# Kernel optimization log

Measured on AMD Instinct MI355X. Metric: run time of the kernel, lower is better.

Reference implementation:

```python
import jax, jax.numpy as jnp
import numpy as np

HEADS = 4
DIM_U = 1
DIM_K = 16
DIM_V = 32  # dim_out // heads = 128 // 4
EPS = 1e-5


def setup_inputs() -> dict:
    key = jax.random.key(0)
    ks = jax.random.split(key, 9)
    b, dim, hh, ww = 16, 256, 32, 32
    n = m = hh * ww
    x = jax.random.normal(ks[0], (b, dim, hh, ww), dtype=jnp.float32)
    # 1x1 conv weights (out_ch, in_ch), kaiming-ish scale
    s = 1.0 / np.sqrt(dim)
    w_q = jax.random.normal(ks[1], (DIM_K * HEADS, dim), dtype=jnp.float32) * s
    w_k = jax.random.normal(ks[2], (DIM_K * DIM_U, dim), dtype=jnp.float32) * s
    w_v = jax.random.normal(ks[3], (DIM_V * DIM_U, dim), dtype=jnp.float32) * s
    pos_emb = jax.random.normal(ks[4], (n, m, DIM_K, DIM_U), dtype=jnp.float32)
    gamma_q = jnp.ones((DIM_K * HEADS,), dtype=jnp.float32)
    beta_q = jnp.zeros((DIM_K * HEADS,), dtype=jnp.float32)
    gamma_v = jnp.ones((DIM_V * DIM_U,), dtype=jnp.float32)
    beta_v = jnp.zeros((DIM_V * DIM_U,), dtype=jnp.float32)
    return {"x": x, "w_q": w_q, "w_k": w_k, "w_v": w_v, "pos_emb": pos_emb,
            "gamma_q": gamma_q, "beta_q": beta_q, "gamma_v": gamma_v, "beta_v": beta_v}


def _bn(t, gamma, beta):
    # BatchNorm2d in training mode: batch statistics over (b, h, w), biased var
    mean = t.mean(axis=(0, 2, 3), keepdims=True)
    var = t.var(axis=(0, 2, 3), keepdims=True)
    t = (t - mean) * jax.lax.rsqrt(var + EPS)
    return t * gamma[None, :, None, None] + beta[None, :, None, None]


def reference(x, w_q, w_k, w_v, pos_emb, gamma_q, beta_q, gamma_v, beta_v):
    b, c, hh, ww = x.shape
    h, u, dk, dv = HEADS, DIM_U, DIM_K, DIM_V
    # 1x1 convs == channel contractions
    q = jnp.einsum('oc,bcxy->boxy', w_q, x)
    k = jnp.einsum('oc,bcxy->boxy', w_k, x)
    v = jnp.einsum('oc,bcxy->boxy', w_v, x)
    q = _bn(q, gamma_q, beta_q)
    v = _bn(v, gamma_v, beta_v)
    n = hh * ww
    q = q.reshape(b, h, dk, n)        # b h k n
    k = k.reshape(b, dk, u, n)        # b k u m
    v = v.reshape(b, dv, u, n)        # b v u m
    k = jax.nn.softmax(k, axis=-1)
    lam_c = jnp.einsum('bkum,bvum->bkv', k, v)            # content lambda
    lam_p = jnp.einsum('nmku,bvum->bnkv', pos_emb, v)     # position lambdas
    Yc = jnp.einsum('bhkn,bkv->bnhv', q, lam_c)
    Yp = jnp.einsum('bhkn,bnkv->bnhv', q, lam_p)
    Y = Yc + Yp                                           # b n h v
    out = Y.transpose(0, 2, 3, 1).reshape(b, h * dv, hh, ww)
    return out
```

## Files before the change

### kernel.cpp

```cpp
#include <hip/hip_runtime.h>
#include <hip/hip_bf16.h>
#include <cstdint>


typedef __attribute__((ext_vector_type(8))) __bf16 bf16x8;
typedef __attribute__((ext_vector_type(4))) float f32x4;

__device__ __forceinline__ unsigned short f2bf(float f) {
    unsigned u = __float_as_uint(f);
    u += 0x7fffu + ((u >> 16) & 1u);
    return (unsigned short)(u >> 16);
}
__device__ __forceinline__ unsigned pk2(float a, float b) {
    return (unsigned)f2bf(a) | ((unsigned)f2bf(b) << 16);
}
__device__ __forceinline__ float bf2f(unsigned short h) {
    return __uint_as_float(((unsigned)h) << 16);
}
__device__ __forceinline__ void async16(const void* g, void* l) {
    __builtin_amdgcn_global_load_lds(
        (const __attribute__((address_space(1))) void*)g,
        (__attribute__((address_space(3))) void*)l, 16, 0, 0);
}

__global__ __launch_bounds__(256) void k_proj(const float* __restrict__ x,
                                              const float* __restrict__ wq,
                                              const float* __restrict__ wk,
                                              const float* __restrict__ wv,
                                              float* __restrict__ qraw,
                                              float* __restrict__ kraw,
                                              float* __restrict__ vraw) {
    int b = blockIdx.y;
    int px0 = blockIdx.x * 32;
    int t = threadIdx.x;
    int w = t >> 6, lane = t & 63;

    __shared__ __align__(16) unsigned short Al[128 * 32];
    __shared__ __align__(16) unsigned short Bl[32 * 34];

    int ch = t >> 1, half = t & 1;
    const float* wsrc = nullptr;
    if (ch < 64)       wsrc = wq + ch * 256;
    else if (ch < 80)  wsrc = wk + (ch - 64) * 256;
    else if (ch < 112) wsrc = wv + (ch - 80) * 256;
    if (wsrc) wsrc += half * 16;
    int s2 = (ch >> 1) & 3;
    unsigned short* wdst0 = &Al[ch * 32 + (((half * 2) ^ s2) << 3)];
    unsigned short* wdst1 = &Al[ch * 32 + (((half * 2 + 1) ^ s2) << 3)];

    int wm = w >> 1, wn = w & 1;
    int rl = lane & 15, qq = lane >> 4;
    int sw = qq ^ ((rl >> 1) & 3);

    f32x4 acc[4];
#pragma unroll
    for (int i = 0; i < 4; ++i)
#pragma unroll
        for (int r = 0; r < 4; ++r) acc[i][r] = 0.f;

    const float* xb = x + (size_t)b * 262144 + px0;

    for (int kt = 0; kt < 8; ++kt) {
        int c0 = kt * 32;
        {
            uint4 d0, d1;
            if (wsrc) {
                float4 f0 = *(const float4*)(wsrc + c0);
                float4 f1 = *(const float4*)(wsrc + c0 + 4);
                float4 f2 = *(const float4*)(wsrc + c0 + 8);
                float4 f3 = *(const float4*)(wsrc + c0 + 12);
                d0.x = pk2(f0.x, f0.y); d0.y = pk2(f0.z, f0.w);
                d0.z = pk2(f1.x, f1.y); d0.w = pk2(f1.z, f1.w);
                d1.x = pk2(f2.x, f2.y); d1.y = pk2(f2.z, f2.w);
                d1.z = pk2(f3.x, f3.y); d1.w = pk2(f3.z, f3.w);
            } else {
                d0 = make_uint4(0, 0, 0, 0); d1 = d0;
            }
            *(uint4*)wdst0 = d0;
            *(uint4*)wdst1 = d1;
        }
#pragma unroll
        for (int rep = 0; rep < 2; ++rep) {
            int idx = rep * 256 + t;
            int px = idx & 31;
            int cp = idx >> 5;
            int c = c0 + cp * 2;
            float f0 = xb[(size_t)c * 1024 + px];
            float f1 = xb[(size_t)(c + 1) * 1024 + px];
            *(unsigned*)&Bl[px * 34 + cp * 2] = pk2(f0, f1);
        }
        __syncthreads();
        bf16x8 a[4], bb;
#pragma unroll
        for (int i = 0; i < 4; ++i) a[i] = *(const bf16x8*)&Al[((wm << 6) + (i << 4) + rl) * 32 + sw * 8];
        bb = *(const bf16x8*)&Bl[((wn << 4) + rl) * 34 + qq * 8];
#pragma unroll
        for (int i = 0; i < 4; ++i)
            acc[i] = __builtin_amdgcn_mfma_f32_16x16x32_bf16(a[i], bb, acc[i], 0, 0, 0);
        __syncthreads();
    }

#pragma unroll
    for (int i = 0; i < 4; ++i) {
        int px = px0 + (wn << 4) + rl;
#pragma unroll
        for (int r = 0; r < 4; ++r) {
            int c = (wm << 6) + (i << 4) + (qq << 2) + r;
            float val = acc[i][r];
            if (c < 64)       qraw[((size_t)b * 64 + c) * 1024 + px] = val;
            else if (c < 80)  kraw[((size_t)b * 16 + (c - 64)) * 1024 + px] = val;
            else if (c < 112) vraw[((size_t)b * 32 + (c - 80)) * 1024 + px] = val;
        }
    }
}

__global__ __launch_bounds__(1024) void k_mid(const float* __restrict__ qraw,
                                              const float* __restrict__ kraw,
                                              const float* __restrict__ vraw,
                                              const float* __restrict__ gq, const float* __restrict__ bq,
                                              const float* __restrict__ gv, const float* __restrict__ bv,
                                              unsigned short* __restrict__ vbn,
                                              float* __restrict__ scaleArr, float* __restrict__ shiftArr,
                                              float* __restrict__ lamcraw) {
    int bx = blockIdx.x;
    int t = threadIdx.x;
    int w = t >> 6, lane = t & 63;
    __shared__ float redA[16], redB[16];
    __shared__ float bc[2];
    __shared__ float pr[16][32];

    if (bx < 96) {
        int ch = bx;
        const float* base;
        size_t bstride;
        if (ch < 64) { base = qraw + (size_t)ch * 1024; bstride = 65536; }
        else         { base = vraw + (size_t)(ch - 64) * 1024; bstride = 32768; }
        float s = 0.f, ss = 0.f;
#pragma unroll
        for (int b = 0; b < 16; ++b) { float v = base[b * bstride + t]; s += v; ss += v * v; }
#pragma unroll
        for (int off = 32; off; off >>= 1) { s += __shfl_down(s, off); ss += __shfl_down(ss, off); }
        if (lane == 0) { redA[w] = s; redB[w] = ss; }
        __syncthreads();
        if (t == 0) {
            s = 0.f; ss = 0.f;
#pragma unroll
            for (int i = 0; i < 16; ++i) { s += redA[i]; ss += redB[i]; }
            float mean = s * (1.f / 16384.f);
            float var = ss * (1.f / 16384.f) - mean * mean;
            float g, be;
            if (ch < 64) { g = gq[ch]; be = bq[ch]; } else { g = gv[ch - 64]; be = bv[ch - 64]; }
            float sc = g * rsqrtf(var + 1e-5f);
            float sh = be - mean * sc;
            scaleArr[ch] = sc; shiftArr[ch] = sh;
            bc[0] = sc; bc[1] = sh;
        }
        __syncthreads();
        if (ch >= 64) {
            float sc = bc[0], sh = bc[1];
            int vch = ch - 64;
#pragma unroll
            for (int b = 0; b < 16; ++b) {
                size_t idx = ((size_t)b * 32 + vch) * 1024 + t;
                vbn[idx] = f2bf(vraw[idx] * sc + sh);
            }
        }
    } else {
        int idx = bx - 96;
        int b = idx >> 4, kch = idx & 15;
        float xv = kraw[((size_t)b * 16 + kch) * 1024 + t];
        float mx = xv;
#pragma unroll
        for (int off = 32; off; off >>= 1) mx = fmaxf(mx, __shfl_down(mx, off));
        if (lane == 0) redA[w] = mx;
        __syncthreads();
        mx = redA[0];
#pragma unroll
        for (int i = 1; i < 16; ++i) mx = fmaxf(mx, redA[i]);
        float e = __expf(xv - mx);
        float s = e;
#pragma unroll
        for (int off = 32; off; off >>= 1) s += __shfl_down(s, off);
        __syncthreads();
        if (lane == 0) redB[w] = s;
        __syncthreads();
        s = 0.f;
#pragma unroll
        for (int i = 0; i < 16; ++i) s += redB[i];
        float inv = 1.f / s;
        const float* vb = vraw + (size_t)b * 32768;
        for (int v = 0; v < 32; ++v) {
            float p = e * vb[(size_t)v * 1024 + t];
#pragma unroll
            for (int off = 32; off; off >>= 1) p += __shfl_down(p, off);
            if (lane == 0) pr[w][v] = p;
        }
        __syncthreads();
        if (t < 32) {
            float tot = 0.f;
#pragma unroll
            for (int i = 0; i < 16; ++i) tot += pr[i][t];
            lamcraw[((size_t)b * 16 + kch) * 32 + t] = inv * tot;
        }
    }
}

__global__ __launch_bounds__(256, 3) void k_lamp(const float* __restrict__ pos,
                                                 const unsigned short* __restrict__ vbn,
                                                 const float* __restrict__ qraw,
                                                 const float* __restrict__ lamcraw,
                                                 const float* __restrict__ scaleArr,
                                                 const float* __restrict__ shiftArr,
                                                 float* __restrict__ out) {
    int mtile = blockIdx.x;
    int ntile = blockIdx.y;
    int t = threadIdx.x;
    int w = t >> 6, lane = t & 63;

    __shared__ union {
        struct { __align__(16) unsigned short A[128 * 68]; __align__(16) unsigned short B[8192]; } st;
        unsigned short Ybf[128 * 132];
    } sm;

    int nl = t >> 5;
    int k0 = (t >> 3) & 3;
    int am = t & 7;
    const float* pAg = pos + ((size_t)(mtile * 8 + nl)) * 16384 + am * 128 + k0 * 4;

    int srow = t >> 3;
    int jx = (t & 7) ^ (srow & 7);
    const unsigned short* pB = vbn + ((size_t)(ntile * 128) + srow) * 1024 + jx * 8;
    unsigned short* ldsB = &sm.st.B[t * 8];

    int wm = w >> 1, wn = w & 1;
    int rl = lane & 15, qq = lane >> 4;
    int abase[2], bbase[2];
#pragma unroll
    for (int ks = 0; ks < 2; ++ks) {
        abase[ks] = (wm * 64 + rl) * 68 + ((ks * 4 + qq) << 3);
        bbase[ks] = (wn * 64 + rl) * 64 + (((ks * 4 + qq) ^ (rl & 7)) << 3);
    }

    f32x4 acc[4][4];
#pragma unroll
    for (int i = 0; i < 4; ++i)
#pragma unroll
        for (int j = 0; j < 4; ++j)
#pragma unroll
            for (int r = 0; r < 4; ++r) acc[i][j][r] = 0.f;

    for (int kt = 0; kt < 16; ++kt) {
#pragma unroll
        for (int i = 0; i < 4; ++i)
            async16(pB + (size_t)i * 32 * 1024 + kt * 64, ldsB + i * 2048);
        const float* ps = pAg + (size_t)kt * 1024;
#pragma unroll
        for (int h = 0; h < 2; ++h) {
            float4 f0 = *(const float4*)(ps + h * 64);
            float4 f1 = *(const float4*)(ps + h * 64 + 16);
            float4 f2 = *(const float4*)(ps + h * 64 + 32);
            float4 f3 = *(const float4*)(ps + h * 64 + 48);
#pragma unroll
            for (int c = 0; c < 4; ++c) {
                uint2 d;
                d.x = pk2(((const float*)&f0)[c], ((const float*)&f1)[c]);
                d.y = pk2(((const float*)&f2)[c], ((const float*)&f3)[c]);
                int row = nl * 16 + k0 * 4 + c;
                *(uint2*)&sm.st.A[row * 68 + am * 8 + h * 4] = d;
            }
        }
        __syncthreads();
#pragma unroll
        for (int ks = 0; ks < 2; ++ks) {
            bf16x8 a[4], bb[4];
#pragma unroll
            for (int i = 0; i < 4; ++i) a[i]  = *(const bf16x8*)&sm.st.A[abase[ks] + i * 16 * 68];
#pragma unroll
            for (int j = 0; j < 4; ++j) bb[j] = *(const bf16x8*)&sm.st.B[bbase[ks] + j * 1024];
#pragma unroll
            for (int i = 0; i < 4; ++i)
#pragma unroll
                for (int j = 0; j < 4; ++j)
                    acc[i][j] = __builtin_amdgcn_mfma_f32_16x16x32_bf16(a[i], bb[j], acc[i][j], 0, 0, 0);
        }
        __syncthreads();
    }

    int b0 = ntile * 4;
#pragma unroll
    for (int j = 0; j < 4; ++j) {
        int col = (wn << 6) + (j << 4) + rl;
        int bcol = col >> 5, vv = col & 31;
        float scv = scaleArr[64 + vv], shv = shiftArr[64 + vv];
        const float* lc = lamcraw + ((size_t)(b0 + bcol) * 16) * 32 + vv;
#pragma unroll
        for (int i = 0; i < 4; ++i) {
            int row_b = (wm << 6) + (i << 4) + (qq << 2);
#pragma unroll
            for (int r = 0; r < 4; ++r) {
                int row = row_b + r;
                float lamc = scv * lc[(row & 15) * 32] + shv;
                sm.Ybf[row * 132 + col] = f2bf(acc[i][j][r] + lamc);
            }
        }
    }
    __syncthreads();

    int c0 = t * 2;
    int bb2 = c0 >> 7;
    int hh = (c0 >> 5) & 3;
    int v0 = c0 & 31;
    int bglob = b0 + bb2;
    float o0[8], o1[8];
#pragma unroll
    for (int nn = 0; nn < 8; ++nn) { o0[nn] = 0.f; o1[nn] = 0.f; }
    const float* qsrc = qraw + ((size_t)bglob * 64 + hh * 16) * 1024 + mtile * 8;
#pragma unroll
    for (int k = 0; k < 16; ++k) {
        float4 qa = *(const float4*)(qsrc + (size_t)k * 1024);
        float4 qb4 = *(const float4*)(qsrc + (size_t)k * 1024 + 4);
        float sc = scaleArr[hh * 16 + k], sh = shiftArr[hh * 16 + k];
        float qv[8] = {qa.x, qa.y, qa.z, qa.w, qb4.x, qb4.y, qb4.z, qb4.w};
#pragma unroll
        for (int nn = 0; nn < 8; ++nn) {
            float qn = qv[nn] * sc + sh;
            unsigned yp = *(const unsigned*)&sm.Ybf[(nn * 16 + k) * 132 + bb2 * 32 + v0];
            o0[nn] += qn * bf2f((unsigned short)(yp & 0xffff));
            o1[nn] += qn * bf2f((unsigned short)(yp >> 16));
        }
    }
    float* op = out + ((size_t)bglob * 128 + hh * 32 + v0) * 1024 + mtile * 8;
    ((float4*)op)[0] = make_float4(o0[0], o0[1], o0[2], o0[3]);
    ((float4*)op)[1] = make_float4(o0[4], o0[5], o0[6], o0[7]);
    float* op1 = op + 1024;
    ((float4*)op1)[0] = make_float4(o1[0], o1[1], o1[2], o1[3]);
    ((float4*)op1)[1] = make_float4(o1[4], o1[5], o1[6], o1[7]);
}

extern "C" void kernel_launch(void* const* d_in, const int* in_sizes, int n_in,
                              void* d_out, int out_size, void* d_ws, size_t ws_size,
                              hipStream_t stream) {
    const float* x   = (const float*)d_in[0];
    const float* wq  = (const float*)d_in[1];
    const float* wk  = (const float*)d_in[2];
    const float* wv  = (const float*)d_in[3];
    const float* pos = (const float*)d_in[4];
    const float* gq  = (const float*)d_in[5];
    const float* bq  = (const float*)d_in[6];
    const float* gv  = (const float*)d_in[7];
    const float* bv  = (const float*)d_in[8];
    float* out = (float*)d_out;

    char* ws = (char*)d_ws;
    float* qraw          = (float*)(ws);
    float* kraw          = (float*)(ws + 4194304);
    float* vraw          = (float*)(ws + 5242880);
    unsigned short* vbn  = (unsigned short*)(ws + 7340032);
    float* lamcraw       = (float*)(ws + 8388608);
    float* scaleArr      = (float*)(ws + 8421376);
    float* shiftArr      = (float*)(ws + 8421888);

    k_proj<<<dim3(32, 16), dim3(256), 0, stream>>>(x, wq, wk, wv, qraw, kraw, vraw);
    k_mid<<<dim3(352), dim3(1024), 0, stream>>>(qraw, kraw, vraw, gq, bq, gv, bv,
                                                vbn, scaleArr, shiftArr, lamcraw);
    k_lamp<<<dim3(128, 4), dim3(256), 0, stream>>>(pos, vbn, qraw, lamcraw,
                                                   scaleArr, shiftArr, out);
}
```

Baseline: 194.9 us.

## Double-buffer A/B tiles in k_lamp to overlap global loads with MFMA

Converts the k_lamp main loop to a two-stage double-buffered pipeline. The next tile's pos data is loaded into registers and the V tile is fetched asynchronously into the alternate LDS buffer while MFMAs run on the current buffer. The fp32-to-bf16 packing of A happens after the compute, so only one barrier per iteration remains. This doubles LDS use (about 66KB) and drops the occupancy hint of 3 from launch_bounds, which may lower the number of resident blocks.

```diff
diff --git a/kernel.cpp b/kernel.cpp
--- a/kernel.cpp
+++ b/kernel.cpp
@@ -205,32 +205,33 @@
     }
 }
 
-__global__ __launch_bounds__(256, 3) void k_lamp(const float* __restrict__ pos,
-                                                 const unsigned short* __restrict__ vbn,
-                                                 const float* __restrict__ qraw,
-                                                 const float* __restrict__ lamcraw,
-                                                 const float* __restrict__ scaleArr,
-                                                 const float* __restrict__ shiftArr,
-                                                 float* __restrict__ out) {
+__global__ __launch_bounds__(256) void k_lamp(const float* __restrict__ pos,
+                                              const unsigned short* __restrict__ vbn,
+                                              const float* __restrict__ qraw,
+                                              const float* __restrict__ lamcraw,
+                                              const float* __restrict__ scaleArr,
+                                              const float* __restrict__ shiftArr,
+                                              float* __restrict__ out) {
     int mtile = blockIdx.x;
     int ntile = blockIdx.y;
     int t = threadIdx.x;
     int w = t >> 6, lane = t & 63;
 
     __shared__ union {
-        struct { __align__(16) unsigned short A[128 * 68]; __align__(16) unsigned short B[8192]; } st;
-        unsigned short Ybf[128 * 132];
+        __align__(16) unsigned short flat[2 * 16896];
+        __align__(16) unsigned short Ybf[128 * 132];
     } sm;
+    const int BUF = 16896, BOFF = 8704;
 
     int nl = t >> 5;
     int k0 = (t >> 3) & 3;
     int am = t & 7;
     const float* pAg = pos + ((size_t)(mtile * 8 + nl)) * 16384 + am * 128 + k0 * 4;
+    int arow0 = (nl * 16 + k0 * 4) * 68 + am * 8;
 
     int srow = t >> 3;
     int jx = (t & 7) ^ (srow & 7);
     const unsigned short* pB = vbn + ((size_t)(ntile * 128) + srow) * 1024 + jx * 8;
-    unsigned short* ldsB = &sm.st.B[t * 8];
 
     int wm = w >> 1, wn = w & 1;
     int rl = lane & 15, qq = lane >> 4;
@@ -238,7 +239,7 @@
 #pragma unroll
     for (int ks = 0; ks < 2; ++ks) {
         abase[ks] = (wm * 64 + rl) * 68 + ((ks * 4 + qq) << 3);
-        bbase[ks] = (wn * 64 + rl) * 64 + (((ks * 4 + qq) ^ (rl & 7)) << 3);
+        bbase[ks] = BOFF + (wn * 64 + rl) * 64 + (((ks * 4 + qq) ^ (rl & 7)) << 3);
     }
 
     f32x4 acc[4][4];
@@ -249,41 +250,59 @@
 #pragma unroll
             for (int r = 0; r < 4; ++r) acc[i][j][r] = 0.f;
 
-    for (int kt = 0; kt < 16; ++kt) {
+    float4 fl[8];
+
+    auto issueA = [&](int kt) {
+        const float* ps = pAg + (size_t)kt * 1024;
+#pragma unroll
+        for (int i = 0; i < 8; ++i) fl[i] = *(const float4*)(ps + i * 16);
+    };
+    auto issueB = [&](int buf, int kt) {
+        unsigned short* ldsB = &sm.flat[buf * BUF + BOFF + t * 8];
 #pragma unroll
         for (int i = 0; i < 4; ++i)
             async16(pB + (size_t)i * 32 * 1024 + kt * 64, ldsB + i * 2048);
-        const float* ps = pAg + (size_t)kt * 1024;
-#pragma unroll
-        for (int h = 0; h < 2; ++h) {
-            float4 f0 = *(const float4*)(ps + h * 64);
-            float4 f1 = *(const float4*)(ps + h * 64 + 16);
-            float4 f2 = *(const float4*)(ps + h * 64 + 32);
-            float4 f3 = *(const float4*)(ps + h * 64 + 48);
-#pragma unroll
-            for (int c = 0; c < 4; ++c) {
-                uint2 d;
-                d.x = pk2(((const float*)&f0)[c], ((const float*)&f1)[c]);
-                d.y = pk2(((const float*)&f2)[c], ((const float*)&f3)[c]);
-                int row = nl * 16 + k0 * 4 + c;
-                *(uint2*)&sm.st.A[row * 68 + am * 8 + h * 4] = d;
-            }
-        }
-        __syncthreads();
+    };
+    auto packA = [&](int buf) {
+        unsigned short* Ab = &sm.flat[buf * BUF];
+#pragma unroll
+        for (int c = 0; c < 4; ++c) {
+            uint2 d0, d1;
+            d0.x = pk2(((const float*)&fl[0])[c], ((const float*)&fl[1])[c]);
+            d0.y = pk2(((const float*)&fl[2])[c], ((const float*)&fl[3])[c]);
+            d1.x = pk2(((const float*)&fl[4])[c], ((const float*)&fl[5])[c]);
+            d1.y = pk2(((const float*)&fl[6])[c], ((const float*)&fl[7])[c]);
+            *(uint2*)&Ab[arow0 + c * 68] = d0;
+            *(uint2*)&Ab[arow0 + c * 68 + 4] = d1;
+        }
+    };
+
+    issueB(0, 0);
+    issueA(0);
+    packA(0);
+
+    for (int kt = 0; kt < 16; ++kt) {
+        int cur = kt & 1, nxt = cur ^ 1;
+        __syncthreads();
+        if (kt < 15) {
+            issueB(nxt, kt + 1);
+            issueA(kt + 1);
+        }
+        const unsigned short* base = &sm.flat[cur * BUF];
 #pragma unroll
         for (int ks = 0; ks < 2; ++ks) {
             bf16x8 a[4], bb[4];
 #pragma unroll
-            for (int i = 0; i < 4; ++i) a[i]  = *(const bf16x8*)&sm.st.A[abase[ks] + i * 16 * 68];
-#pragma unroll
-            for (int j = 0; j < 4; ++j) bb[j] = *(const bf16x8*)&sm.st.B[bbase[ks] + j * 1024];
+            for (int i = 0; i < 4; ++i) a[i]  = *(const bf16x8*)&base[abase[ks] + i * 16 * 68];
+#pragma unroll
+            for (int j = 0; j < 4; ++j) bb[j] = *(const bf16x8*)&base[bbase[ks] + j * 1024];
 #pragma unroll
             for (int i = 0; i < 4; ++i)
 #pragma unroll
                 for (int j = 0; j < 4; ++j)
                     acc[i][j] = __builtin_amdgcn_mfma_f32_16x16x32_bf16(a[i], bb[j], acc[i][j], 0, 0, 0);
         }
-        __syncthreads();
+        if (kt < 15) packA(nxt);
     }
 
     int b0 = ntile * 4;
```

New measurement: 222.0 us. +13.9%, slower.

## Pre-convert pos_emb to bf16 k-major layout and double-buffer async loads in k_lamp

Applied to the files above, without the earlier changes.

A new front kernel fuses the q/k/v projection with extra blocks that convert pos_emb from fp32 to bf16 and transpose it into a k-major layout in workspace. k_lamp then fetches both operands with async global-to-LDS copies into a two-stage buffer, overlapping the next tile's loads with MFMA work. This replaces the per-tile fp32 loads and register conversions that k_lamp previously repeated for each of its four n-tiles. The Y staging buffer also moves from bf16 to fp32. The cost is an extra 32MB bf16 write and read of pos each call, a larger workspace, and more LDS use in k_lamp.

```diff
diff --git a/kernel.cpp b/kernel.cpp
--- a/kernel.cpp
+++ b/kernel.cpp
@@ -23,20 +23,50 @@
         (__attribute__((address_space(3))) void*)l, 16, 0, 0);
 }
 
-__global__ __launch_bounds__(256) void k_proj(const float* __restrict__ x,
-                                              const float* __restrict__ wq,
-                                              const float* __restrict__ wk,
-                                              const float* __restrict__ wv,
-                                              float* __restrict__ qraw,
-                                              float* __restrict__ kraw,
-                                              float* __restrict__ vraw) {
-    int b = blockIdx.y;
-    int px0 = blockIdx.x * 32;
+__global__ __launch_bounds__(256) void k_front(const float* __restrict__ pos,
+                                               unsigned* __restrict__ PbfU,
+                                               const float* __restrict__ x,
+                                               const float* __restrict__ wq,
+                                               const float* __restrict__ wk,
+                                               const float* __restrict__ wv,
+                                               float* __restrict__ qraw,
+                                               float* __restrict__ kraw,
+                                               float* __restrict__ vraw) {
+    int blk = blockIdx.x;
     int t = threadIdx.x;
+
+    __shared__ union {
+        __align__(16) unsigned short L[16 * 1032];
+        struct { __align__(16) unsigned short Al[128 * 32], Bl[32 * 34]; } pj;
+    } sm;
+
+    if (blk >= 512) {
+        int n = blk - 512;
+        const float4* src = (const float4*)(pos + (size_t)n * 16384);
+#pragma unroll
+        for (int r = 0; r < 16; ++r) {
+            int idx4 = r * 256 + t;
+            float4 f = src[idx4];
+            int m = idx4 >> 2, k0 = (idx4 & 3) << 2;
+            sm.L[(k0 + 0) * 1032 + m] = f2bf(f.x);
+            sm.L[(k0 + 1) * 1032 + m] = f2bf(f.y);
+            sm.L[(k0 + 2) * 1032 + m] = f2bf(f.z);
+            sm.L[(k0 + 3) * 1032 + m] = f2bf(f.w);
+        }
+        __syncthreads();
+        uint2* dst = (uint2*)(PbfU + (size_t)n * 8192);
+#pragma unroll
+        for (int r = 0; r < 16; ++r) {
+            int c = r * 256 + t;
+            int k = c >> 8, mo = c & 255;
+            dst[c] = *(const uint2*)&sm.L[k * 1032 + mo * 4];
+        }
+        return;
+    }
+
+    int b = blk >> 5;
+    int px0 = (blk & 31) * 32;
     int w = t >> 6, lane = t & 63;
-
-    __shared__ __align__(16) unsigned short Al[128 * 32];
-    __shared__ __align__(16) unsigned short Bl[32 * 34];
 
     int ch = t >> 1, half = t & 1;
     const float* wsrc = nullptr;
@@ -45,8 +75,8 @@
     else if (ch < 112) wsrc = wv + (ch - 80) * 256;
     if (wsrc) wsrc += half * 16;
     int s2 = (ch >> 1) & 3;
-    unsigned short* wdst0 = &Al[ch * 32 + (((half * 2) ^ s2) << 3)];
-    unsigned short* wdst1 = &Al[ch * 32 + (((half * 2 + 1) ^ s2) << 3)];
+    unsigned short* wdst0 = &sm.pj.Al[ch * 32 + (((half * 2) ^ s2) << 3)];
+    unsigned short* wdst1 = &sm.pj.Al[ch * 32 + (((half * 2 + 1) ^ s2) << 3)];
 
     int wm = w >> 1, wn = w & 1;
     int rl = lane & 15, qq = lane >> 4;
@@ -87,13 +117,13 @@
             int c = c0 + cp * 2;
             float f0 = xb[(size_t)c * 1024 + px];
             float f1 = xb[(size_t)(c + 1) * 1024 + px];
-            *(unsigned*)&Bl[px * 34 + cp * 2] = pk2(f0, f1);
+            *(unsigned*)&sm.pj.Bl[px * 34 + cp * 2] = pk2(f0, f1);
         }
         __syncthreads();
         bf16x8 a[4], bb;
 #pragma unroll
-        for (int i = 0; i < 4; ++i) a[i] = *(const bf16x8*)&Al[((wm << 6) + (i << 4) + rl) * 32 + sw * 8];
-        bb = *(const bf16x8*)&Bl[((wn << 4) + rl) * 34 + qq * 8];
+        for (int i = 0; i < 4; ++i) a[i] = *(const bf16x8*)&sm.pj.Al[((wm << 6) + (i << 4) + rl) * 32 + sw * 8];
+        bb = *(const bf16x8*)&sm.pj.Bl[((wn << 4) + rl) * 34 + qq * 8];
 #pragma unroll
         for (int i = 0; i < 4; ++i)
             acc[i] = __builtin_amdgcn_mfma_f32_16x16x32_bf16(a[i], bb, acc[i], 0, 0, 0);
@@ -205,41 +235,47 @@
     }
 }
 
-__global__ __launch_bounds__(256, 3) void k_lamp(const float* __restrict__ pos,
-                                                 const unsigned short* __restrict__ vbn,
-                                                 const float* __restrict__ qraw,
-                                                 const float* __restrict__ lamcraw,
-                                                 const float* __restrict__ scaleArr,
-                                                 const float* __restrict__ shiftArr,
-                                                 float* __restrict__ out) {
+__global__ __launch_bounds__(256) void k_lamp(const unsigned short* __restrict__ Pbf,
+                                              const unsigned short* __restrict__ vbn,
+                                              const float* __restrict__ qraw,
+                                              const float* __restrict__ lamcraw,
+                                              const float* __restrict__ scaleArr,
+                                              const float* __restrict__ shiftArr,
+                                              float* __restrict__ out) {
     int mtile = blockIdx.x;
     int ntile = blockIdx.y;
     int t = threadIdx.x;
     int w = t >> 6, lane = t & 63;
 
     __shared__ union {
-        struct { __align__(16) unsigned short A[128 * 68]; __align__(16) unsigned short B[8192]; } st;
-        unsigned short Ybf[128 * 132];
+        __align__(16) unsigned short st[4][8192];
+        float Y[128 * 128];
     } sm;
 
-    int nl = t >> 5;
-    int k0 = (t >> 3) & 3;
-    int am = t & 7;
-    const float* pAg = pos + ((size_t)(mtile * 8 + nl)) * 16384 + am * 128 + k0 * 4;
-
-    int srow = t >> 3;
-    int jx = (t & 7) ^ (srow & 7);
-    const unsigned short* pB = vbn + ((size_t)(ntile * 128) + srow) * 1024 + jx * 8;
-    unsigned short* ldsB = &sm.st.B[t * 8];
+    int roff = lane >> 3;
+    int jx = (lane & 7) ^ (roff & 7);
+    const unsigned short* pA[4];
+    const unsigned short* pB[4];
+#pragma unroll
+    for (int i = 0; i < 4; ++i) {
+        int rowA = mtile * 128 + w * 32 + i * 8 + roff;
+        int rowB = ntile * 128 + w * 32 + i * 8 + roff;
+        pA[i] = Pbf + (size_t)rowA * 1024 + jx * 8;
+        pB[i] = vbn + (size_t)rowB * 1024 + jx * 8;
+    }
 
     int wm = w >> 1, wn = w & 1;
     int rl = lane & 15, qq = lane >> 4;
-    int abase[2], bbase[2];
-#pragma unroll
-    for (int ks = 0; ks < 2; ++ks) {
-        abase[ks] = (wm * 64 + rl) * 68 + ((ks * 4 + qq) << 3);
-        bbase[ks] = (wn * 64 + rl) * 64 + (((ks * 4 + qq) ^ (rl & 7)) << 3);
-    }
+    int aoff[2][4], boff[2][4];
+#pragma unroll
+    for (int ks = 0; ks < 2; ++ks)
+#pragma unroll
+        for (int i = 0; i < 4; ++i) {
+            int rowA = wm * 64 + i * 16 + rl;
+            aoff[ks][i] = rowA * 64 + (((ks * 4 + qq) ^ (rowA & 7)) << 3);
+            int rowB = wn * 64 + i * 16 + rl;
+            boff[ks][i] = rowB * 64 + (((ks * 4 + qq) ^ (rowB & 7)) << 3);
+        }
 
     f32x4 acc[4][4];
 #pragma unroll
@@ -249,34 +285,31 @@
 #pragma unroll
             for (int r = 0; r < 4; ++r) acc[i][j][r] = 0.f;
 
+    auto stage = [&](int s, int kk) {
+        unsigned short* dstA = &sm.st[s][0];
+        unsigned short* dstB = &sm.st[s + 1][0];
+#pragma unroll
+        for (int i = 0; i < 4; ++i) {
+            async16(pA[i] + kk * 64, dstA + w * 2048 + i * 512);
+            async16(pB[i] + kk * 64, dstB + w * 2048 + i * 512);
+        }
+    };
+
+    stage(0, 0);
+    __syncthreads();
+
     for (int kt = 0; kt < 16; ++kt) {
-#pragma unroll
-        for (int i = 0; i < 4; ++i)
-            async16(pB + (size_t)i * 32 * 1024 + kt * 64, ldsB + i * 2048);
-        const float* ps = pAg + (size_t)kt * 1024;
-#pragma unroll
-        for (int h = 0; h < 2; ++h) {
-            float4 f0 = *(const float4*)(ps + h * 64);
-            float4 f1 = *(const float4*)(ps + h * 64 + 16);
-            float4 f2 = *(const float4*)(ps + h * 64 + 32);
-            float4 f3 = *(const float4*)(ps + h * 64 + 48);
-#pragma unroll
-            for (int c = 0; c < 4; ++c) {
-                uint2 d;
-                d.x = pk2(((const float*)&f0)[c], ((const float*)&f1)[c]);
-                d.y = pk2(((const float*)&f2)[c], ((const float*)&f3)[c]);
-                int row = nl * 16 + k0 * 4 + c;
-                *(uint2*)&sm.st.A[row * 68 + am * 8 + h * 4] = d;
-            }
-        }
-        __syncthreads();
+        int cur = (kt & 1) ? 2 : 0;
+        if (kt < 15) stage(cur ^ 2, kt + 1);
+        const unsigned short* curA = &sm.st[cur][0];
+        const unsigned short* curB = &sm.st[cur + 1][0];
 #pragma unroll
         for (int ks = 0; ks < 2; ++ks) {
             bf16x8 a[4], bb[4];
 #pragma unroll
-            for (int i = 0; i < 4; ++i) a[i]  = *(const bf16x8*)&sm.st.A[abase[ks] + i * 16 * 68];
-#pragma unroll
-            for (int j = 0; j < 4; ++j) bb[j] = *(const bf16x8*)&sm.st.B[bbase[ks] + j * 1024];
+            for (int i = 0; i < 4; ++i) a[i]  = *(const bf16x8*)&curA[aoff[ks][i]];
+#pragma unroll
+            for (int j = 0; j < 4; ++j) bb[j] = *(const bf16x8*)&curB[boff[ks][j]];
 #pragma unroll
             for (int i = 0; i < 4; ++i)
 #pragma unroll
@@ -299,8 +332,7 @@
 #pragma unroll
             for (int r = 0; r < 4; ++r) {
                 int row = row_b + r;
-                float lamc = scv * lc[(row & 15) * 32] + shv;
-                sm.Ybf[row * 132 + col] = f2bf(acc[i][j][r] + lamc);
+                sm.Y[row * 128 + col] = acc[i][j][r] + scv * lc[(row & 15) * 32] + shv;
             }
         }
     }
@@ -321,12 +353,12 @@
         float4 qb4 = *(const float4*)(qsrc + (size_t)k * 1024 + 4);
         float sc = scaleArr[hh * 16 + k], sh = shiftArr[hh * 16 + k];
         float qv[8] = {qa.x, qa.y, qa.z, qa.w, qb4.x, qb4.y, qb4.z, qb4.w};
+        const float* yrow = &sm.Y[k * 128 + bb2 * 32 + v0];
 #pragma unroll
         for (int nn = 0; nn < 8; ++nn) {
             float qn = qv[nn] * sc + sh;
-            unsigned yp = *(const unsigned*)&sm.Ybf[(nn * 16 + k) * 132 + bb2 * 32 + v0];
-            o0[nn] += qn * bf2f((unsigned short)(yp & 0xffff));
-            o1[nn] += qn * bf2f((unsigned short)(yp >> 16));
+            o0[nn] += qn * yrow[nn * 16 * 128];
+            o1[nn] += qn * yrow[nn * 16 * 128 + 1];
         }
     }
     float* op = out + ((size_t)bglob * 128 + hh * 32 + v0) * 1024 + mtile * 8;
@@ -352,17 +384,19 @@
     float* out = (float*)d_out;
 
     char* ws = (char*)d_ws;
-    float* qraw          = (float*)(ws);
-    float* kraw          = (float*)(ws + 4194304);
-    float* vraw          = (float*)(ws + 5242880);
-    unsigned short* vbn  = (unsigned short*)(ws + 7340032);
-    float* lamcraw       = (float*)(ws + 8388608);
-    float* scaleArr      = (float*)(ws + 8421376);
-    float* shiftArr      = (float*)(ws + 8421888);
-
-    k_proj<<<dim3(32, 16), dim3(256), 0, stream>>>(x, wq, wk, wv, qraw, kraw, vraw);
+    unsigned short* Pbf  = (unsigned short*)(ws);
+    float* qraw          = (float*)(ws + 33554432);
+    float* kraw          = (float*)(ws + 37748736);
+    float* vraw          = (float*)(ws + 38797312);
+    unsigned short* vbn  = (unsigned short*)(ws + 40894464);
+    float* lamcraw       = (float*)(ws + 41943040);
+    float* scaleArr      = (float*)(ws + 41975808);
+    float* shiftArr      = (float*)(ws + 41976320);
+
+    k_front<<<dim3(1536), dim3(256), 0, stream>>>(pos, (unsigned*)Pbf, x, wq, wk, wv,
+                                                  qraw, kraw, vraw);
     k_mid<<<dim3(352), dim3(1024), 0, stream>>>(qraw, kraw, vraw, gq, bq, gv, bv,
                                                 vbn, scaleArr, shiftArr, lamcraw);
-    k_lamp<<<dim3(128, 4), dim3(256), 0, stream>>>(pos, vbn, qraw, lamcraw,
+    k_lamp<<<dim3(128, 4), dim3(256), 0, stream>>>(Pbf, vbn, qraw, lamcraw,
                                                    scaleArr, shiftArr, out);
 }
```

New measurement: 182.9 us. -6.2%, faster.
